# Kernel tuning notes

Hardware: AMD Instinct MI355X
Metric: run time of the kernel (lower is better)

## Reference

```python
import jax, jax.numpy as jnp
import numpy as np

DELAYS = (1, 2, 4, 8, 16, 32)


def setup_inputs() -> dict:
    key = jax.random.key(0)
    embeddings = jax.random.normal(key, (4, 4096, 1024), dtype=jnp.float32)
    return {"embeddings": embeddings}


def reference(embeddings) -> jnp.ndarray:
    # embeddings: [B, S, D]. For each delay d: out_d[t] = emb[t-d] if t >= d else emb[t].
    # (buffer_size=64 >= max delay, so the circular buffer is equivalent to plain shifts.)
    B, S, D = embeddings.shape
    t = jnp.arange(S)
    outs = []
    for d in DELAYS:
        shifted = jnp.roll(embeddings, d, axis=1)          # wrapped values masked out below
        valid = (t >= d)[None, :, None]                    # [1, S, 1]
        outs.append(jnp.where(valid, shifted, embeddings))
    return jnp.concatenate(outs, axis=-1)                  # [B, S, 6*D]
```

## Files before the change

kernel.cpp:

```cpp
#include <hip/hip_runtime.h>


constexpr unsigned B = 4;
constexpr unsigned S = 4096;
constexpr unsigned D = 1024;
constexpr unsigned ND = 6;
constexpr unsigned D4 = D / 4;

__global__ __launch_bounds__(256) void delay_buffer_kernel(
    const float4* __restrict__ in, float4* __restrict__ out) {
    const unsigned bid = blockIdx.x;
    const unsigned di  = bid % ND;
    const unsigned bt  = bid / ND;
    const unsigned t   = bt & (S - 1);
    const unsigned d   = 1u << di;
    const unsigned src_bt = (t >= d) ? (bt - d) : bt;

    out[(size_t)bid * D4 + threadIdx.x] = in[(size_t)src_bt * D4 + threadIdx.x];
}

extern "C" void kernel_launch(void* const* d_in, const int* in_sizes, int n_in,
                              void* d_out, int out_size, void* d_ws, size_t ws_size,
                              hipStream_t stream) {
    const float4* in  = (const float4*)d_in[0];
    float4*       out = (float4*)d_out;

    const unsigned grid = B * S * ND;
    delay_buffer_kernel<<<grid, 256, 0, stream>>>(in, out);
}
```

Baseline: 467.6 us.

## Scatter each input row once to all delay outputs with persistent grid

```diff
diff --git a/kernel.cpp b/kernel.cpp
--- a/kernel.cpp
+++ b/kernel.cpp
@@ -1,30 +1,37 @@
 #include <hip/hip_runtime.h>
 
 
-constexpr unsigned B = 4;
-constexpr unsigned S = 4096;
-constexpr unsigned D = 1024;
+using f32x4 = __attribute__((ext_vector_type(4))) float;
+
+constexpr unsigned B  = 4;
+constexpr unsigned S  = 4096;
 constexpr unsigned ND = 6;
-constexpr unsigned D4 = D / 4;
+constexpr unsigned D4 = 1024 / 4;
+constexpr unsigned NROWS = B * S;
 
-__global__ __launch_bounds__(256) void delay_buffer_kernel(
-    const float4* __restrict__ in, float4* __restrict__ out) {
-    const unsigned bid = blockIdx.x;
-    const unsigned di  = bid % ND;
-    const unsigned bt  = bid / ND;
-    const unsigned t   = bt & (S - 1);
-    const unsigned d   = 1u << di;
-    const unsigned src_bt = (t >= d) ? (bt - d) : bt;
-
-    out[(size_t)bid * D4 + threadIdx.x] = in[(size_t)src_bt * D4 + threadIdx.x];
+__global__ __launch_bounds__(256) void delay_scatter(
+    const f32x4* __restrict__ in, f32x4* __restrict__ out) {
+    const unsigned tid = threadIdx.x;
+    for (unsigned row = blockIdx.x; row < NROWS; row += gridDim.x) {
+        const unsigned t = row & (S - 1);
+        const f32x4 v = __builtin_nontemporal_load(&in[(size_t)row * D4 + tid]);
+        const size_t ob = (size_t)row * (ND * D4) + tid;
+        #pragma unroll
+        for (unsigned di = 0; di < ND; ++di) {
+            const unsigned d = 1u << di;
+            if (t + d < S)
+                __builtin_nontemporal_store(v, &out[ob + (size_t)(d * ND + di) * D4]);
+            if (t < d)
+                __builtin_nontemporal_store(v, &out[ob + (size_t)di * D4]);
+        }
+    }
 }
 
 extern "C" void kernel_launch(void* const* d_in, const int* in_sizes, int n_in,
                               void* d_out, int out_size, void* d_ws, size_t ws_size,
                               hipStream_t stream) {
-    const float4* in  = (const float4*)d_in[0];
-    float4*       out = (float4*)d_out;
+    const f32x4* in  = (const f32x4*)d_in[0];
+    f32x4*       out = (f32x4*)d_out;
 
-    const unsigned grid = B * S * ND;
-    delay_buffer_kernel<<<grid, 256, 0, stream>>>(in, out);
+    delay_scatter<<<2048, 256, 0, stream>>>(in, out);
 }
```

New measurement: 433.8 us. 1.08x faster.
